# Kernel tuning notes

Hardware: AMD Instinct MI355X
Metric: run time of the kernel (lower is better)

## Reference

```python
import jax, jax.numpy as jnp
import numpy as np

TOKEN_DIM = 192
NUM_HEADS = 4
HEAD_DIM = TOKEN_DIM // NUM_HEADS
TOPK = 128


def _pos_enc(H, W, td):
    # 2D sinusoidal PE identical to GlobalMatcher._get_position_encoding -> [H*W, td]
    y = jnp.repeat(jnp.arange(H, dtype=jnp.float32), W)
    x = jnp.tile(jnp.arange(W, dtype=jnp.float32), H)
    dh = td // 2
    div = jnp.exp(jnp.arange(dh, dtype=jnp.float32) * (-np.log(10000.0) / dh))
    pe_sin = jnp.sin(x[:, None] * div)                       # [N, dh]
    pe_cos = jnp.cos(y[:, None] * div[: td - dh])            # [N, td-dh]
    return jnp.concatenate([pe_sin, pe_cos], axis=1)


def _matcher(feat1, feat2, qw, qb, kw, kb, vw, vb, ow, ob):
    # EfficientGlobalMatcher forward (chunking is a memory detail; math == full topk)
    B, C, H, W = feat1.shape
    N = H * W
    f1 = feat1.reshape(B, C, N).transpose(0, 2, 1)           # [B, N, C]
    f2 = feat2.reshape(B, C, N).transpose(0, 2, 1)
    Q = f1 @ qw + qb                                          # [B, N, td]
    K = f2 @ kw + kb
    V = f2 @ vw + vb
    pe = _pos_enc(H, W, TOKEN_DIM)
    Q = Q + pe[None]
    K = K + pe[None]
    def split(t):  # [B, N, h*d] -> [B, h, N, d]
        return t.reshape(B, N, NUM_HEADS, HEAD_DIM).transpose(0, 2, 1, 3)
    Qh, Kh, Vh = split(Q), split(K), split(V)
    scale = 1.0 / np.sqrt(HEAD_DIM)
    scores = jnp.einsum('bhnd,bhmd->bhnm', Qh, Kh) * scale    # [B, h, N, N]
    k = min(TOPK, N)
    top_vals, top_idx = jax.lax.top_k(scores, k)              # [B, h, N, k]
    attn = jax.nn.softmax(top_vals, axis=-1)
    # gather V rows per (b, h, query, k): [B, h, N, k, d]
    Vg = jnp.take_along_axis(Vh[:, :, None, :, :], top_idx[..., None], axis=3)
    out = jnp.einsum('bhnk,bhnkd->bhnd', attn, Vg)            # [B, h, N, d]
    out = out.transpose(0, 2, 1, 3).reshape(B, N, TOKEN_DIM)
    out = out @ ow + ob
    return out.transpose(0, 2, 1).reshape(B, TOKEN_DIM, H, W)


def setup_inputs() -> dict:
    key = jax.random.key(0)
    dims = [64, 128, 192]
    shapes = [(2, 64, 64, 64), (2, 128, 32, 32), (2, 192, 16, 16)]
    inp = {}
    ks = jax.random.split(key, 32)
    ki = 0
    for lvl, shp in enumerate(shapes):
        inp[f'feat1_{lvl}'] = jax.random.normal(ks[ki], shp, jnp.float32); ki += 1
        inp[f'feat2_{lvl}'] = jax.random.normal(ks[ki], shp, jnp.float32); ki += 1
    for lvl, d in enumerate(dims):
        for nm in ('q', 'k', 'v'):
            inp[f'{nm}w{lvl}'] = jax.random.normal(ks[ki], (d, TOKEN_DIM), jnp.float32) * 0.02; ki += 1
            inp[f'{nm}b{lvl}'] = jnp.zeros((TOKEN_DIM,), jnp.float32)
        inp[f'ow{lvl}'] = jax.random.normal(ks[ki], (TOKEN_DIM, TOKEN_DIM), jnp.float32) * 0.02; ki += 1
        inp[f'ob{lvl}'] = jnp.zeros((TOKEN_DIM,), jnp.float32)
    return inp


def reference(feat1_0, feat2_0, feat1_1, feat2_1, feat1_2, feat2_2,
              qw0, qb0, kw0, kb0, vw0, vb0, ow0, ob0,
              qw1, qb1, kw1, kb1, vw1, vb1, ow1, ob1,
              qw2, qb2, kw2, kb2, vw2, vb2, ow2, ob2):
    t0 = _matcher(feat1_0, feat2_0, qw0, qb0, kw0, kb0, vw0, vb0, ow0, ob0)
    t1 = _matcher(feat1_1, feat2_1, qw1, qb1, kw1, kb1, vw1, vb1, ow1, ob1)
    t2 = _matcher(feat1_2, feat2_2, qw2, qb2, kw2, kb2, vw2, vb2, ow2, ob2)
    return (t0, t1, t2)
```

## Files before the change

### kernel.cpp

```cpp
#include <hip/hip_runtime.h>
#include <math.h>

#define TD 192
#define HD 48
#define KSEL 128
#define QB 4

__device__ __forceinline__ unsigned f2o(float f) {
  unsigned u = __float_as_uint(f);
  return (u & 0x80000000u) ? ~u : (u | 0x80000000u);
}
__device__ __forceinline__ float o2f(unsigned u) {
  unsigned v = (u & 0x80000000u) ? (u & 0x7fffffffu) : ~u;
  return __uint_as_float(v);
}

__global__ void pe_kernel(float* __restrict__ pe, int W) {
  int n = blockIdx.x;
  int t = threadIdx.x;
  const float c = -0.09594104554885301f;
  float val;
  if (t < 96) {
    float dv = expf((float)t * c);
    val = sinf((float)(n % W) * dv);
  } else {
    float dv = expf((float)(t - 96) * c);
    val = cosf((float)(n / W) * dv);
  }
  pe[n * TD + t] = val;
}

__global__ __launch_bounds__(256) void qkv_tiled(
    const float* __restrict__ feat1, const float* __restrict__ feat2,
    const float* __restrict__ qw, const float* __restrict__ qb,
    const float* __restrict__ kw, const float* __restrict__ kb,
    const float* __restrict__ vw, const float* __restrict__ vb,
    const float* __restrict__ pe,
    float* __restrict__ Q, float* __restrict__ Kt, float* __restrict__ V,
    int C, int N) {
  __shared__ float ftile[64][64];
  const int type = blockIdx.y;
  const int tid = threadIdx.x;
  const int gtok = blockIdx.x * 64;
  const int b = gtok / N, n0 = gtok - b * N;
  const float* feat = (type == 0) ? feat1 : feat2;
  const float* wsel = (type == 0) ? qw : (type == 1) ? kw : vw;
  const float* bsel = (type == 0) ? qb : (type == 1) ? kb : vb;
  const int cg = tid >> 4, tg = tid & 15;
  const int ch0 = cg * 12, t0 = tg * 4;

  float4 z = make_float4(0.f, 0.f, 0.f, 0.f);
  float4 a0 = z, a1 = z, a2 = z, a3 = z, a4 = z, a5 = z,
         a6 = z, a7 = z, a8 = z, a9 = z, a10 = z, a11 = z;

  for (int c0 = 0; c0 < C; c0 += 64) {
#pragma unroll
    for (int rep = 0; rep < 4; ++rep) {
      int off = rep * 1024 + tid * 4;
      int r = off >> 6, cc = off & 63;
      *reinterpret_cast<float4*>(&ftile[r][cc]) =
          *reinterpret_cast<const float4*>(&feat[((size_t)(b * C + c0 + r)) * N + n0 + cc]);
    }
    __syncthreads();
#pragma unroll 8
    for (int k = 0; k < 64; ++k) {
      float4 f4 = *reinterpret_cast<const float4*>(&ftile[k][t0]);
      const float* wr = wsel + (size_t)(c0 + k) * TD + ch0;
      float4 w0 = *reinterpret_cast<const float4*>(wr);
      float4 w1 = *reinterpret_cast<const float4*>(wr + 4);
      float4 w2 = *reinterpret_cast<const float4*>(wr + 8);
#define QFMA(A, WS) A.x = fmaf(WS, f4.x, A.x); A.y = fmaf(WS, f4.y, A.y); \
                    A.z = fmaf(WS, f4.z, A.z); A.w = fmaf(WS, f4.w, A.w);
      QFMA(a0, w0.x) QFMA(a1, w0.y) QFMA(a2, w0.z) QFMA(a3, w0.w)
      QFMA(a4, w1.x) QFMA(a5, w1.y) QFMA(a6, w1.z) QFMA(a7, w1.w)
      QFMA(a8, w2.x) QFMA(a9, w2.y) QFMA(a10, w2.z) QFMA(a11, w2.w)
#undef QFMA
    }
    __syncthreads();
  }
  {
    float4 b0 = *reinterpret_cast<const float4*>(&bsel[ch0]);
    float4 b1 = *reinterpret_cast<const float4*>(&bsel[ch0 + 4]);
    float4 b2 = *reinterpret_cast<const float4*>(&bsel[ch0 + 8]);
#define BADD(A, S) A.x += S; A.y += S; A.z += S; A.w += S;
    BADD(a0, b0.x) BADD(a1, b0.y) BADD(a2, b0.z) BADD(a3, b0.w)
    BADD(a4, b1.x) BADD(a5, b1.y) BADD(a6, b1.z) BADD(a7, b1.w)
    BADD(a8, b2.x) BADD(a9, b2.y) BADD(a10, b2.z) BADD(a11, b2.w)
#undef BADD
  }
  if (type < 2) {
#define PEADD(F, TT) { \
    const float* pr = pe + (size_t)(n0 + t0 + (TT)) * TD + ch0; \
    float4 p0 = *reinterpret_cast<const float4*>(pr); \
    float4 p1 = *reinterpret_cast<const float4*>(pr + 4); \
    float4 p2 = *reinterpret_cast<const float4*>(pr + 8); \
    a0.F += p0.x; a1.F += p0.y; a2.F += p0.z; a3.F += p0.w; \
    a4.F += p1.x; a5.F += p1.y; a6.F += p1.z; a7.F += p1.w; \
    a8.F += p2.x; a9.F += p2.y; a10.F += p2.z; a11.F += p2.w; }
    PEADD(x, 0) PEADD(y, 1) PEADD(z, 2) PEADD(w, 3)
#undef PEADD
  }
  if (type == 1) {
#define KSTORE(A, CI) { int ch = ch0 + (CI); int h = ch / HD, d = ch - h * HD; \
    *reinterpret_cast<float4*>(&Kt[((size_t)(b * 4 + h) * HD + d) * N + n0 + t0]) = A; }
    KSTORE(a0, 0) KSTORE(a1, 1) KSTORE(a2, 2) KSTORE(a3, 3)
    KSTORE(a4, 4) KSTORE(a5, 5) KSTORE(a6, 6) KSTORE(a7, 7)
    KSTORE(a8, 8) KSTORE(a9, 9) KSTORE(a10, 10) KSTORE(a11, 11)
#undef KSTORE
  } else {
    float* out = (type == 0) ? Q : V;
#define RSTORE(F, TT) { \
    float* orow = out + (size_t)(b * N + n0 + t0 + (TT)) * TD + ch0; \
    *reinterpret_cast<float4*>(orow)     = make_float4(a0.F, a1.F, a2.F, a3.F); \
    *reinterpret_cast<float4*>(orow + 4) = make_float4(a4.F, a5.F, a6.F, a7.F); \
    *reinterpret_cast<float4*>(orow + 8) = make_float4(a8.F, a9.F, a10.F, a11.F); }
    RSTORE(x, 0) RSTORE(y, 1) RSTORE(z, 2) RSTORE(w, 3)
#undef RSTORE
  }
}

template <int N, int RK, bool FUSE>
__global__ __launch_bounds__(256) void attnA_kernel(
    const float* __restrict__ Q, const float* __restrict__ Kt,
    unsigned* __restrict__ ckey, unsigned short* __restrict__ cidx,
    const float* __restrict__ V, float* __restrict__ O, int bh0) {
  constexpr int R = N / RK;
  constexpr int NV4 = RK / 256;
  constexpr int nq = N / QB;
  constexpr int NCOPY = RK / 256;
  __shared__ unsigned sb[QB * RK];
  __shared__ float qv[QB][HD];

  const int tid = threadIdx.x;
  const int r = blockIdx.x % R;
  const int qg = (blockIdx.x / R) % nq;
  const int bhloc = blockIdx.x / (R * nq);
  const int bh = bh0 + bhloc;
  const int b = bh >> 2, h = bh & 3;
  const int q0 = qg * QB;
  const float scale = 0.14433756729740643f;

  if (tid < QB * HD) {
    int q = tid / HD, d = tid - q * HD;
    qv[q][d] = Q[((size_t)(b * N + q0 + q)) * TD + h * HD + d];
  }
  __syncthreads();

  const int w = tid >> 6, lane = tid & 63;
  const unsigned long long lanelt = (1ull << lane) - 1ull;
  const float* kt = Kt + ((size_t)(b * 4 + h) * HD) * N + r * RK;

  for (int j0 = tid * 4; j0 < RK; j0 += 1024) {
    float4 acc[QB];
#pragma unroll
    for (int q = 0; q < QB; ++q) acc[q] = make_float4(0.f, 0.f, 0.f, 0.f);
#pragma unroll
    for (int d4 = 0; d4 < HD; d4 += 4) {
      float4 k0 = *reinterpret_cast<const float4*>(kt + (size_t)(d4 + 0) * N + j0);
      float4 k1 = *reinterpret_cast<const float4*>(kt + (size_t)(d4 + 1) * N + j0);
      float4 k2 = *reinterpret_cast<const float4*>(kt + (size_t)(d4 + 2) * N + j0);
      float4 k3 = *reinterpret_cast<const float4*>(kt + (size_t)(d4 + 3) * N + j0);
#pragma unroll
      for (int q = 0; q < QB; ++q) {
        float4 qq = *reinterpret_cast<const float4*>(&qv[q][d4]);
        acc[q].x = fmaf(qq.x, k0.x, acc[q].x); acc[q].x = fmaf(qq.y, k1.x, acc[q].x);
        acc[q].x = fmaf(qq.z, k2.x, acc[q].x); acc[q].x = fmaf(qq.w, k3.x, acc[q].x);
        acc[q].y = fmaf(qq.x, k0.y, acc[q].y); acc[q].y = fmaf(qq.y, k1.y, acc[q].y);
        acc[q].y = fmaf(qq.z, k2.y, acc[q].y); acc[q].y = fmaf(qq.w, k3.y, acc[q].y);
        acc[q].z = fmaf(qq.x, k0.z, acc[q].z); acc[q].z = fmaf(qq.y, k1.z, acc[q].z);
        acc[q].z = fmaf(qq.z, k2.z, acc[q].z); acc[q].z = fmaf(qq.w, k3.z, acc[q].z);
        acc[q].w = fmaf(qq.x, k0.w, acc[q].w); acc[q].w = fmaf(qq.y, k1.w, acc[q].w);
        acc[q].w = fmaf(qq.z, k2.w, acc[q].w); acc[q].w = fmaf(qq.w, k3.w, acc[q].w);
      }
    }
#pragma unroll
    for (int q = 0; q < QB; ++q) {
      uint4 kk;
      kk.x = f2o(acc[q].x * scale); kk.y = f2o(acc[q].y * scale);
      kk.z = f2o(acc[q].z * scale); kk.w = f2o(acc[q].w * scale);
      *reinterpret_cast<uint4*>(&sb[q * RK + j0]) = kk;
    }
  }
  __syncthreads();

  uint4 kr[NV4];
#pragma unroll
  for (int i = 0; i < NV4; ++i)
    kr[i] = *reinterpret_cast<const uint4*>(&sb[w * RK + i * 256 + lane * 4]);

  unsigned* h4 = sb + w * RK;
  const unsigned cb = ((unsigned)lane & (NCOPY - 1u)) << 8;
  const unsigned cx = ((unsigned)lane & (NCOPY - 1u)) << 3;

  unsigned kth = 0u, mask = 0u;
  int rem = KSEL;
#pragma unroll
  for (int shift = 24; shift >= 0; shift -= 8) {
#pragma unroll
    for (int i = 0; i < NCOPY; ++i)
      *reinterpret_cast<uint4*>(&h4[i * 256 + lane * 4]) = make_uint4(0, 0, 0, 0);
    if (shift == 24) {
#pragma unroll
      for (int i = 0; i < NV4; ++i) {
        atomicAdd(&h4[cb + (((kr[i].x >> 24)) ^ cx)], 1u);
        atomicAdd(&h4[cb + (((kr[i].y >> 24)) ^ cx)], 1u);
        atomicAdd(&h4[cb + (((kr[i].z >> 24)) ^ cx)], 1u);
        atomicAdd(&h4[cb + (((kr[i].w >> 24)) ^ cx)], 1u);
      }
    } else {
#pragma unroll
      for (int i = 0; i < NV4; ++i) {
        if ((kr[i].x & mask) == kth) atomicAdd(&h4[cb + (((kr[i].x >> shift) & 255u) ^ cx)], 1u);
        if ((kr[i].y & mask) == kth) atomicAdd(&h4[cb + (((kr[i].y >> shift) & 255u) ^ cx)], 1u);
        if ((kr[i].z & mask) == kth) atomicAdd(&h4[cb + (((kr[i].z >> shift) & 255u) ^ cx)], 1u);
        if ((kr[i].w & mask) == kth) atomicAdd(&h4[cb + (((kr[i].w >> shift) & 255u) ^ cx)], 1u);
      }
    }
    int v[4], loc = 0;
#pragma unroll
    for (int i = 0; i < 4; ++i) {
      unsigned bin = (unsigned)(255 - (lane * 4 + i));
      unsigned s = 0;
#pragma unroll
      for (int c = 0; c < NCOPY; ++c) s += h4[c * 256 + (bin ^ ((unsigned)c << 3))];
      v[i] = (int)s;
      loc += v[i];
    }
    int incl = loc;
#pragma unroll
    for (int off = 1; off < 64; off <<= 1) {
      int t = __shfl_up(incl, off, 64);
      if (lane >= off) incl += t;
    }
    int c = incl - loc;
    int selidx = -1, selexcl = 0;
#pragma unroll
    for (int i = 0; i < 4; ++i) {
      if (selidx < 0 && rem > c && rem <= c + v[i]) {
        selidx = 255 - (lane * 4 + i); selexcl = c;
      }
      c += v[i];
    }
    unsigned long long vote = __ballot(selidx >= 0);
    int src = __ffsll((long long)vote) - 1;
    selidx = __shfl(selidx, src, 64);
    selexcl = __shfl(selexcl, src, 64);
    rem -= selexcl;
    kth |= ((unsigned)selidx << shift);
    mask |= (0xFFu << shift);
  }
  const int need_eq = rem;

  if constexpr (FUSE) {
    unsigned mk = 0u;
#pragma unroll
    for (int i = 0; i < NV4; ++i) {
      unsigned a_ = kr[i].x > kr[i].y ? kr[i].x : kr[i].y;
      unsigned b_ = kr[i].z > kr[i].w ? kr[i].z : kr[i].w;
      a_ = a_ > b_ ? a_ : b_; mk = a_ > mk ? a_ : mk;
    }
    for (int off = 32; off > 0; off >>= 1) {
      unsigned o = (unsigned)__shfl_xor((int)mk, off, 64);
      mk = o > mk ? o : mk;
    }
    const float mx = o2f(mk);

    __shared__ int idxb[4][KSEL];
    __shared__ float wb[4][KSEL];
    int selbase = 0, eqbase = 0;
    float lz = 0.f;
#pragma unroll
    for (int i = 0; i < NV4; ++i) {
      const int jb = i * 256 + lane * 4;
      const unsigned u0 = kr[i].x, u1 = kr[i].y, u2 = kr[i].z, u3 = kr[i].w;
      const bool e0 = (u0 == kth), e1 = (u1 == kth), e2 = (u2 == kth), e3 = (u3 == kth);
      const unsigned long long b0 = __ballot(e0), b1 = __ballot(e1), b2 = __ballot(e2), b3 = __ballot(e3);
      const int eqlt = __popcll(b0 & lanelt) + __popcll(b1 & lanelt) + __popcll(b2 & lanelt) + __popcll(b3 & lanelt);
      int eo = 0;
      const bool s0 = (u0 > kth) || (e0 && (eqbase + eqlt + eo) < need_eq); eo += e0 ? 1 : 0;
      const bool s1 = (u1 > kth) || (e1 && (eqbase + eqlt + eo) < need_eq); eo += e1 ? 1 : 0;
      const bool s2 = (u2 > kth) || (e2 && (eqbase + eqlt + eo) < need_eq); eo += e2 ? 1 : 0;
      const bool s3 = (u3 > kth) || (e3 && (eqbase + eqlt + eo) < need_eq); eo += e3 ? 1 : 0;
      const unsigned long long c0 = __ballot(s0), c1 = __ballot(s1), c2 = __ballot(s2), c3 = __ballot(s3);
      const int sellt = __popcll(c0 & lanelt) + __popcll(c1 & lanelt) + __popcll(c2 & lanelt) + __popcll(c3 & lanelt);
      int so = 0;
      if (s0) { int p = selbase + sellt + so; float e = expf(o2f(u0) - mx); idxb[w][p] = jb + 0; wb[w][p] = e; lz += e; } so += s0 ? 1 : 0;
      if (s1) { int p = selbase + sellt + so; float e = expf(o2f(u1) - mx); idxb[w][p] = jb + 1; wb[w][p] = e; lz += e; } so += s1 ? 1 : 0;
      if (s2) { int p = selbase + sellt + so; float e = expf(o2f(u2) - mx); idxb[w][p] = jb + 2; wb[w][p] = e; lz += e; } so += s2 ? 1 : 0;
      if (s3) { int p = selbase + sellt + so; float e = expf(o2f(u3) - mx); idxb[w][p] = jb + 3; wb[w][p] = e; lz += e; } so += s3 ? 1 : 0;
      eqbase += __popcll(b0) + __popcll(b1) + __popcll(b2) + __popcll(b3);
      selbase += __popcll(c0) + __popcll(c1) + __popcll(c2) + __popcll(c3);
    }
    for (int off = 32; off > 0; off >>= 1) lz += __shfl_xor(lz, off, 64);
    const float rz = 1.f / lz;
    if (lane < HD) {
      float acc = 0.f;
#pragma unroll 4
      for (int p = 0; p < KSEL; ++p) {
        acc = fmaf(wb[w][p], V[((size_t)(b * N + idxb[w][p])) * TD + h * HD + lane], acc);
      }
      O[((size_t)(b * N + q0 + w)) * TD + h * HD + lane] = acc * rz;
    }
  } else {
    unsigned* ok = ckey + (((size_t)bhloc * N + q0 + w) * R + r) * KSEL;
    unsigned short* oi = cidx + (((size_t)bhloc * N + q0 + w) * R + r) * KSEL;
    int selbase = 0, eqbase = 0;
#pragma unroll
    for (int i = 0; i < NV4; ++i) {
      const int jb = r * RK + i * 256 + lane * 4;
      const unsigned u0 = kr[i].x, u1 = kr[i].y, u2 = kr[i].z, u3 = kr[i].w;
      const bool e0 = (u0 == kth), e1 = (u1 == kth), e2 = (u2 == kth), e3 = (u3 == kth);
      const unsigned long long b0 = __ballot(e0), b1 = __ballot(e1), b2 = __ballot(e2), b3 = __ballot(e3);
      const int eqlt = __popcll(b0 & lanelt) + __popcll(b1 & lanelt) + __popcll(b2 & lanelt) + __popcll(b3 & lanelt);
      int eo = 0;
      const bool s0 = (u0 > kth) || (e0 && (eqbase + eqlt + eo) < need_eq); eo += e0 ? 1 : 0;
      const bool s1 = (u1 > kth) || (e1 && (eqbase + eqlt + eo) < need_eq); eo += e1 ? 1 : 0;
      const bool s2 = (u2 > kth) || (e2 && (eqbase + eqlt + eo) < need_eq); eo += e2 ? 1 : 0;
      const bool s3 = (u3 > kth) || (e3 && (eqbase + eqlt + eo) < need_eq); eo += e3 ? 1 : 0;
      const unsigned long long c0 = __ballot(s0), c1 = __ballot(s1), c2 = __ballot(s2), c3 = __ballot(s3);
      const int sellt = __popcll(c0 & lanelt) + __popcll(c1 & lanelt) + __popcll(c2 & lanelt) + __popcll(c3 & lanelt);
      int so = 0;
      if (s0) { int p = selbase + sellt + so; ok[p] = u0; oi[p] = (unsigned short)(jb + 0); } so += s0 ? 1 : 0;
      if (s1) { int p = selbase + sellt + so; ok[p] = u1; oi[p] = (unsigned short)(jb + 1); } so += s1 ? 1 : 0;
      if (s2) { int p = selbase + sellt + so; ok[p] = u2; oi[p] = (unsigned short)(jb + 2); } so += s2 ? 1 : 0;
      if (s3) { int p = selbase + sellt + so; ok[p] = u3; oi[p] = (unsigned short)(jb + 3); } so += s3 ? 1 : 0;
      eqbase += __popcll(b0) + __popcll(b1) + __popcll(b2) + __popcll(b3);
      selbase += __popcll(c0) + __popcll(c1) + __popcll(c2) + __popcll(c3);
    }
  }
}

template <int CN>
__global__ __launch_bounds__(256) void attnB_kernel(
    const unsigned* __restrict__ ckey, const unsigned short* __restrict__ cidx,
    const float* __restrict__ V, float* __restrict__ O, int N, int bh0) {
  constexpr int CL = CN / 64;
  __shared__ unsigned hist[4][256];
  __shared__ int idxb[4][KSEL];
  __shared__ float wb[4][KSEL];

  const int tid = threadIdx.x, w = tid >> 6, lane = tid & 63;
  const unsigned long long lanelt = (1ull << lane) - 1ull;
  const int g = blockIdx.x * 4 + w;
  const int bhloc = g / N;
  const int qi = g - bhloc * N;
  const int bh = bh0 + bhloc;
  const int b = bh >> 2, h = bh & 3;

  unsigned ck[CL], ci[CL];
#pragma unroll
  for (int i = 0; i < CL; ++i) {
    ck[i] = ckey[(size_t)g * CN + i * 64 + lane];
    ci[i] = cidx[(size_t)g * CN + i * 64 + lane];
  }

  unsigned mk = 0u;
#pragma unroll
  for (int i = 0; i < CL; ++i) mk = ck[i] > mk ? ck[i] : mk;
  for (int off = 32; off > 0; off >>= 1) {
    unsigned o = (unsigned)__shfl_xor((int)mk, off, 64);
    mk = o > mk ? o : mk;
  }
  const float mx = o2f(mk);

  unsigned* hw = hist[w];
  unsigned kth = 0u, mask = 0u;
  int rem = KSEL;
#pragma unroll
  for (int shift = 24; shift >= 0; shift -= 8) {
#pragma unroll
    for (int i = 0; i < 4; ++i) hw[lane + i * 64] = 0u;
#pragma unroll
    for (int i = 0; i < CL; ++i)
      if ((ck[i] & mask) == kth) atomicAdd(&hw[(ck[i] >> shift) & 255u], 1u);
    int v[4], loc = 0;
#pragma unroll
    for (int i = 0; i < 4; ++i) { v[i] = (int)hw[255 - (lane * 4 + i)]; loc += v[i]; }
    int incl = loc;
#pragma unroll
    for (int off = 1; off < 64; off <<= 1) {
      int t = __shfl_up(incl, off, 64);
      if (lane >= off) incl += t;
    }
    int c = incl - loc;
    int selidx = -1, selexcl = 0;
#pragma unroll
    for (int i = 0; i < 4; ++i) {
      if (selidx < 0 && rem > c && rem <= c + v[i]) {
        selidx = 255 - (lane * 4 + i); selexcl = c;
      }
      c += v[i];
    }
    unsigned long long vote = __ballot(selidx >= 0);
    int src = __ffsll((long long)vote) - 1;
    selidx = __shfl(selidx, src, 64);
    selexcl = __shfl(selexcl, src, 64);
    rem -= selexcl;
    kth |= ((unsigned)selidx << shift);
    mask |= (0xFFu << shift);
  }
  const int need_eq = rem;

  int selbase = 0, eqbase = 0;
  float lz = 0.f;
#pragma unroll
  for (int i = 0; i < CL; ++i) {
    const unsigned u = ck[i];
    const bool eq = (u == kth);
    const unsigned long long beq = __ballot(eq);
    const int eqrank = eqbase + __popcll(beq & lanelt);
    const bool sel = (u > kth) || (eq && eqrank < need_eq);
    const unsigned long long bsel = __ballot(sel);
    const int pos = selbase + __popcll(bsel & lanelt);
    if (sel) {
      float e = expf(o2f(u) - mx);
      idxb[w][pos] = (int)ci[i];
      wb[w][pos] = e;
      lz += e;
    }
    eqbase += __popcll(beq);
    selbase += __popcll(bsel);
  }
  for (int off = 32; off > 0; off >>= 1) lz += __shfl_xor(lz, off, 64);
  const float rz = 1.f / lz;

  if (lane < HD) {
    float acc = 0.f;
#pragma unroll 4
    for (int p = 0; p < KSEL; ++p) {
      acc = fmaf(wb[w][p], V[((size_t)(b * N + idxb[w][p])) * TD + h * HD + lane], acc);
    }
    O[((size_t)(b * N + qi)) * TD + h * HD + lane] = acc * rz;
  }
}

#define OTOK 16
__global__ __launch_bounds__(256) void oproj_kernel(
    const float* __restrict__ O, const float* __restrict__ ow,
    const float* __restrict__ ob, float* __restrict__ out, int N) {
  __shared__ float otile[OTOK][TD + 1];
  const int tid = threadIdx.x;
  const int nt = N / OTOK;
  const int b = blockIdx.x / nt;
  const int n0 = (blockIdx.x % nt) * OTOK;
  const float* obase = O + ((size_t)(b * N + n0)) * TD;
  for (int idx = tid * 4; idx < OTOK * TD; idx += 1024) {
    float4 v = *reinterpret_cast<const float4*>(obase + idx);
    int r = idx / TD, c = idx - r * TD;
    otile[r][c] = v.x; otile[r][c + 1] = v.y; otile[r][c + 2] = v.z; otile[r][c + 3] = v.w;
  }
  __syncthreads();
  const int nl = tid & 15;
  const int ts = (tid >> 4) * 12;
  float a0 = 0.f, a1 = 0.f, a2 = 0.f, a3 = 0.f, a4 = 0.f, a5 = 0.f,
        a6 = 0.f, a7 = 0.f, a8 = 0.f, a9 = 0.f, a10 = 0.f, a11 = 0.f;
  for (int c = 0; c < TD; ++c) {
    float oval = otile[nl][c];
    const float* wr = ow + c * TD + ts;
    float4 w0 = *reinterpret_cast<const float4*>(wr);
    float4 w1 = *reinterpret_cast<const float4*>(wr + 4);
    float4 w2 = *reinterpret_cast<const float4*>(wr + 8);
    a0 = fmaf(oval, w0.x, a0); a1 = fmaf(oval, w0.y, a1);
    a2 = fmaf(oval, w0.z, a2); a3 = fmaf(oval, w0.w, a3);
    a4 = fmaf(oval, w1.x, a4); a5 = fmaf(oval, w1.y, a5);
    a6 = fmaf(oval, w1.z, a6); a7 = fmaf(oval, w1.w, a7);
    a8 = fmaf(oval, w2.x, a8); a9 = fmaf(oval, w2.y, a9);
    a10 = fmaf(oval, w2.z, a10); a11 = fmaf(oval, w2.w, a11);
  }
  const size_t ob2 = ((size_t)b * TD + ts) * N + n0 + nl;
  out[ob2 + 0 * N] = a0 + ob[ts + 0];
  out[ob2 + 1 * N] = a1 + ob[ts + 1];
  out[ob2 + 2 * N] = a2 + ob[ts + 2];
  out[ob2 + 3 * N] = a3 + ob[ts + 3];
  out[ob2 + 4 * N] = a4 + ob[ts + 4];
  out[ob2 + 5 * N] = a5 + ob[ts + 5];
  out[ob2 + 6 * N] = a6 + ob[ts + 6];
  out[ob2 + 7 * N] = a7 + ob[ts + 7];
  out[ob2 + 8 * N] = a8 + ob[ts + 8];
  out[ob2 + 9 * N] = a9 + ob[ts + 9];
  out[ob2 + 10 * N] = a10 + ob[ts + 10];
  out[ob2 + 11 * N] = a11 + ob[ts + 11];
}

extern "C" void kernel_launch(void* const* d_in, const int* in_sizes, int n_in,
                              void* d_out, int out_size, void* d_ws, size_t ws_size,
                              hipStream_t stream) {
  const int B = 2;
  const int Cs[3] = {64, 128, 192};
  const int Hs[3] = {64, 32, 16};
  const size_t out_off[3] = {0,
                             (size_t)2 * TD * 64 * 64,
                             (size_t)2 * TD * 64 * 64 + (size_t)2 * TD * 32 * 32};

  float* ws = (float*)d_ws;
  float* pe = ws;
  float* Q = pe + (size_t)4096 * TD;
  float* Kt = Q + (size_t)B * 4096 * TD;
  float* V = Kt + (size_t)B * 4096 * TD;
  float* Obuf = V + (size_t)B * 4096 * TD;
  unsigned* ckey = (unsigned*)(Obuf + (size_t)B * 4096 * TD);
  unsigned short* cidx = (unsigned short*)(ckey + (size_t)2 * 4096 * 512);

  for (int lvl = 0; lvl < 3; ++lvl) {
    int C = Cs[lvl], H = Hs[lvl], W = H, N = H * W;
    const float* feat1 = (const float*)d_in[lvl * 2 + 0];
    const float* feat2 = (const float*)d_in[lvl * 2 + 1];
    const float* qw = (const float*)d_in[6 + lvl * 8 + 0];
    const float* qb = (const float*)d_in[6 + lvl * 8 + 1];
    const float* kw = (const float*)d_in[6 + lvl * 8 + 2];
    const float* kb = (const float*)d_in[6 + lvl * 8 + 3];
    const float* vw = (const float*)d_in[6 + lvl * 8 + 4];
    const float* vb = (const float*)d_in[6 + lvl * 8 + 5];
    const float* ow = (const float*)d_in[6 + lvl * 8 + 6];
    const float* ob = (const float*)d_in[6 + lvl * 8 + 7];

    pe_kernel<<<N, TD, 0, stream>>>(pe, W);
    dim3 gq(B * N / 64, 3);
    qkv_tiled<<<gq, 256, 0, stream>>>(feat1, feat2, qw, qb, kw, kb, vw, vb, pe, Q, Kt, V, C, N);

    if (N == 4096) {
      for (int g = 0; g < 4; ++g) {
        attnA_kernel<4096, 1024, false><<<8192, 256, 0, stream>>>(
            Q, Kt, ckey, cidx, V, Obuf, g * 2);
        attnB_kernel<512><<<2 * 4096 / 4, 256, 0, stream>>>(
            ckey, cidx, V, Obuf, 4096, g * 2);
      }
    } else if (N == 1024) {
      attnA_kernel<1024, 1024, true><<<8 * 256, 256, 0, stream>>>(
          Q, Kt, ckey, cidx, V, Obuf, 0);
    } else {
      attnA_kernel<256, 256, true><<<8 * 64, 256, 0, stream>>>(
          Q, Kt, ckey, cidx, V, Obuf, 0);
    }
    oproj_kernel<<<B * (N / OTOK), 256, 0, stream>>>(Obuf, ow, ob, (float*)d_out + out_off[lvl], N);
  }
}
```

Measured before the change: 971.0 us.

## Add tie-free fast path to top-k selection, single-copy refine histograms, larger head groups

```diff
diff --git a/kernel.cpp b/kernel.cpp
--- a/kernel.cpp
+++ b/kernel.cpp
@@ -193,38 +193,41 @@
   const unsigned cx = ((unsigned)lane & (NCOPY - 1u)) << 3;
 
   unsigned kth = 0u, mask = 0u;
-  int rem = KSEL;
+  int rem = KSEL, eqcnt = 0;
 #pragma unroll
   for (int shift = 24; shift >= 0; shift -= 8) {
-#pragma unroll
-    for (int i = 0; i < NCOPY; ++i)
-      *reinterpret_cast<uint4*>(&h4[i * 256 + lane * 4]) = make_uint4(0, 0, 0, 0);
+    int v[4], loc = 0;
     if (shift == 24) {
 #pragma unroll
+      for (int i = 0; i < NCOPY; ++i)
+        *reinterpret_cast<uint4*>(&h4[i * 256 + lane * 4]) = make_uint4(0, 0, 0, 0);
+#pragma unroll
       for (int i = 0; i < NV4; ++i) {
-        atomicAdd(&h4[cb + (((kr[i].x >> 24)) ^ cx)], 1u);
-        atomicAdd(&h4[cb + (((kr[i].y >> 24)) ^ cx)], 1u);
-        atomicAdd(&h4[cb + (((kr[i].z >> 24)) ^ cx)], 1u);
-        atomicAdd(&h4[cb + (((kr[i].w >> 24)) ^ cx)], 1u);
+        atomicAdd(&h4[cb + ((kr[i].x >> 24) ^ cx)], 1u);
+        atomicAdd(&h4[cb + ((kr[i].y >> 24) ^ cx)], 1u);
+        atomicAdd(&h4[cb + ((kr[i].z >> 24) ^ cx)], 1u);
+        atomicAdd(&h4[cb + ((kr[i].w >> 24) ^ cx)], 1u);
+      }
+#pragma unroll
+      for (int i = 0; i < 4; ++i) {
+        unsigned bin = (unsigned)(255 - (lane * 4 + i));
+        unsigned s = 0;
+#pragma unroll
+        for (int c = 0; c < NCOPY; ++c) s += h4[c * 256 + (bin ^ ((unsigned)c << 3))];
+        v[i] = (int)s;
+        loc += v[i];
       }
     } else {
+      *reinterpret_cast<uint4*>(&h4[lane * 4]) = make_uint4(0, 0, 0, 0);
 #pragma unroll
       for (int i = 0; i < NV4; ++i) {
-        if ((kr[i].x & mask) == kth) atomicAdd(&h4[cb + (((kr[i].x >> shift) & 255u) ^ cx)], 1u);
-        if ((kr[i].y & mask) == kth) atomicAdd(&h4[cb + (((kr[i].y >> shift) & 255u) ^ cx)], 1u);
-        if ((kr[i].z & mask) == kth) atomicAdd(&h4[cb + (((kr[i].z >> shift) & 255u) ^ cx)], 1u);
-        if ((kr[i].w & mask) == kth) atomicAdd(&h4[cb + (((kr[i].w >> shift) & 255u) ^ cx)], 1u);
-      }
-    }
-    int v[4], loc = 0;
-#pragma unroll
-    for (int i = 0; i < 4; ++i) {
-      unsigned bin = (unsigned)(255 - (lane * 4 + i));
-      unsigned s = 0;
-#pragma unroll
-      for (int c = 0; c < NCOPY; ++c) s += h4[c * 256 + (bin ^ ((unsigned)c << 3))];
-      v[i] = (int)s;
-      loc += v[i];
+        if ((kr[i].x & mask) == kth) atomicAdd(&h4[(kr[i].x >> shift) & 255u], 1u);
+        if ((kr[i].y & mask) == kth) atomicAdd(&h4[(kr[i].y >> shift) & 255u], 1u);
+        if ((kr[i].z & mask) == kth) atomicAdd(&h4[(kr[i].z >> shift) & 255u], 1u);
+        if ((kr[i].w & mask) == kth) atomicAdd(&h4[(kr[i].w >> shift) & 255u], 1u);
+      }
+#pragma unroll
+      for (int i = 0; i < 4; ++i) { v[i] = (int)h4[255 - (lane * 4 + i)]; loc += v[i]; }
     }
     int incl = loc;
 #pragma unroll
@@ -233,11 +236,11 @@
       if (lane >= off) incl += t;
     }
     int c = incl - loc;
-    int selidx = -1, selexcl = 0;
+    int selidx = -1, selexcl = 0, selval = 0;
 #pragma unroll
     for (int i = 0; i < 4; ++i) {
       if (selidx < 0 && rem > c && rem <= c + v[i]) {
-        selidx = 255 - (lane * 4 + i); selexcl = c;
+        selidx = 255 - (lane * 4 + i); selexcl = c; selval = v[i];
       }
       c += v[i];
     }
@@ -245,11 +248,13 @@
     int src = __ffsll((long long)vote) - 1;
     selidx = __shfl(selidx, src, 64);
     selexcl = __shfl(selexcl, src, 64);
+    eqcnt = __shfl(selval, src, 64);
     rem -= selexcl;
     kth |= ((unsigned)selidx << shift);
     mask |= (0xFFu << shift);
   }
   const int need_eq = rem;
+  const bool simple = (eqcnt == need_eq);
 
   if constexpr (FUSE) {
     unsigned mk = 0u;
@@ -267,29 +272,47 @@
 
     __shared__ int idxb[4][KSEL];
     __shared__ float wb[4][KSEL];
-    int selbase = 0, eqbase = 0;
     float lz = 0.f;
-#pragma unroll
-    for (int i = 0; i < NV4; ++i) {
-      const int jb = i * 256 + lane * 4;
-      const unsigned u0 = kr[i].x, u1 = kr[i].y, u2 = kr[i].z, u3 = kr[i].w;
-      const bool e0 = (u0 == kth), e1 = (u1 == kth), e2 = (u2 == kth), e3 = (u3 == kth);
-      const unsigned long long b0 = __ballot(e0), b1 = __ballot(e1), b2 = __ballot(e2), b3 = __ballot(e3);
-      const int eqlt = __popcll(b0 & lanelt) + __popcll(b1 & lanelt) + __popcll(b2 & lanelt) + __popcll(b3 & lanelt);
-      int eo = 0;
-      const bool s0 = (u0 > kth) || (e0 && (eqbase + eqlt + eo) < need_eq); eo += e0 ? 1 : 0;
-      const bool s1 = (u1 > kth) || (e1 && (eqbase + eqlt + eo) < need_eq); eo += e1 ? 1 : 0;
-      const bool s2 = (u2 > kth) || (e2 && (eqbase + eqlt + eo) < need_eq); eo += e2 ? 1 : 0;
-      const bool s3 = (u3 > kth) || (e3 && (eqbase + eqlt + eo) < need_eq); eo += e3 ? 1 : 0;
-      const unsigned long long c0 = __ballot(s0), c1 = __ballot(s1), c2 = __ballot(s2), c3 = __ballot(s3);
-      const int sellt = __popcll(c0 & lanelt) + __popcll(c1 & lanelt) + __popcll(c2 & lanelt) + __popcll(c3 & lanelt);
-      int so = 0;
-      if (s0) { int p = selbase + sellt + so; float e = expf(o2f(u0) - mx); idxb[w][p] = jb + 0; wb[w][p] = e; lz += e; } so += s0 ? 1 : 0;
-      if (s1) { int p = selbase + sellt + so; float e = expf(o2f(u1) - mx); idxb[w][p] = jb + 1; wb[w][p] = e; lz += e; } so += s1 ? 1 : 0;
-      if (s2) { int p = selbase + sellt + so; float e = expf(o2f(u2) - mx); idxb[w][p] = jb + 2; wb[w][p] = e; lz += e; } so += s2 ? 1 : 0;
-      if (s3) { int p = selbase + sellt + so; float e = expf(o2f(u3) - mx); idxb[w][p] = jb + 3; wb[w][p] = e; lz += e; } so += s3 ? 1 : 0;
-      eqbase += __popcll(b0) + __popcll(b1) + __popcll(b2) + __popcll(b3);
-      selbase += __popcll(c0) + __popcll(c1) + __popcll(c2) + __popcll(c3);
+    if (simple) {
+      int selbase = 0;
+#pragma unroll
+      for (int i = 0; i < NV4; ++i) {
+        const int jb = i * 256 + lane * 4;
+        const unsigned u0 = kr[i].x, u1 = kr[i].y, u2 = kr[i].z, u3 = kr[i].w;
+        const bool s0 = (u0 >= kth), s1 = (u1 >= kth), s2 = (u2 >= kth), s3 = (u3 >= kth);
+        const unsigned long long c0 = __ballot(s0), c1 = __ballot(s1), c2 = __ballot(s2), c3 = __ballot(s3);
+        const int sellt = __popcll(c0 & lanelt) + __popcll(c1 & lanelt) + __popcll(c2 & lanelt) + __popcll(c3 & lanelt);
+        int so = 0;
+        if (s0) { int p = selbase + sellt + so; float e = expf(o2f(u0) - mx); idxb[w][p] = jb + 0; wb[w][p] = e; lz += e; } so += s0 ? 1 : 0;
+        if (s1) { int p = selbase + sellt + so; float e = expf(o2f(u1) - mx); idxb[w][p] = jb + 1; wb[w][p] = e; lz += e; } so += s1 ? 1 : 0;
+        if (s2) { int p = selbase + sellt + so; float e = expf(o2f(u2) - mx); idxb[w][p] = jb + 2; wb[w][p] = e; lz += e; } so += s2 ? 1 : 0;
+        if (s3) { int p = selbase + sellt + so; float e = expf(o2f(u3) - mx); idxb[w][p] = jb + 3; wb[w][p] = e; lz += e; } so += s3 ? 1 : 0;
+        selbase += __popcll(c0) + __popcll(c1) + __popcll(c2) + __popcll(c3);
+      }
+    } else {
+      int selbase = 0, eqbase = 0;
+#pragma unroll
+      for (int i = 0; i < NV4; ++i) {
+        const int jb = i * 256 + lane * 4;
+        const unsigned u0 = kr[i].x, u1 = kr[i].y, u2 = kr[i].z, u3 = kr[i].w;
+        const bool e0 = (u0 == kth), e1 = (u1 == kth), e2 = (u2 == kth), e3 = (u3 == kth);
+        const unsigned long long b0 = __ballot(e0), b1 = __ballot(e1), b2 = __ballot(e2), b3 = __ballot(e3);
+        const int eqlt = __popcll(b0 & lanelt) + __popcll(b1 & lanelt) + __popcll(b2 & lanelt) + __popcll(b3 & lanelt);
+        int eo = 0;
+        const bool s0 = (u0 > kth) || (e0 && (eqbase + eqlt + eo) < need_eq); eo += e0 ? 1 : 0;
+        const bool s1 = (u1 > kth) || (e1 && (eqbase + eqlt + eo) < need_eq); eo += e1 ? 1 : 0;
+        const bool s2 = (u2 > kth) || (e2 && (eqbase + eqlt + eo) < need_eq); eo += e2 ? 1 : 0;
+        const bool s3 = (u3 > kth) || (e3 && (eqbase + eqlt + eo) < need_eq); eo += e3 ? 1 : 0;
+        const unsigned long long c0 = __ballot(s0), c1 = __ballot(s1), c2 = __ballot(s2), c3 = __ballot(s3);
+        const int sellt = __popcll(c0 & lanelt) + __popcll(c1 & lanelt) + __popcll(c2 & lanelt) + __popcll(c3 & lanelt);
+        int so = 0;
+        if (s0) { int p = selbase + sellt + so; float e = expf(o2f(u0) - mx); idxb[w][p] = jb + 0; wb[w][p] = e; lz += e; } so += s0 ? 1 : 0;
+        if (s1) { int p = selbase + sellt + so; float e = expf(o2f(u1) - mx); idxb[w][p] = jb + 1; wb[w][p] = e; lz += e; } so += s1 ? 1 : 0;
+        if (s2) { int p = selbase + sellt + so; float e = expf(o2f(u2) - mx); idxb[w][p] = jb + 2; wb[w][p] = e; lz += e; } so += s2 ? 1 : 0;
+        if (s3) { int p = selbase + sellt + so; float e = expf(o2f(u3) - mx); idxb[w][p] = jb + 3; wb[w][p] = e; lz += e; } so += s3 ? 1 : 0;
+        eqbase += __popcll(b0) + __popcll(b1) + __popcll(b2) + __popcll(b3);
+        selbase += __popcll(c0) + __popcll(c1) + __popcll(c2) + __popcll(c3);
+      }
     }
     for (int off = 32; off > 0; off >>= 1) lz += __shfl_xor(lz, off, 64);
     const float rz = 1.f / lz;
@@ -304,28 +327,46 @@
   } else {
     unsigned* ok = ckey + (((size_t)bhloc * N + q0 + w) * R + r) * KSEL;
     unsigned short* oi = cidx + (((size_t)bhloc * N + q0 + w) * R + r) * KSEL;
-    int selbase = 0, eqbase = 0;
-#pragma unroll
-    for (int i = 0; i < NV4; ++i) {
-      const int jb = r * RK + i * 256 + lane * 4;
-      const unsigned u0 = kr[i].x, u1 = kr[i].y, u2 = kr[i].z, u3 = kr[i].w;
-      const bool e0 = (u0 == kth), e1 = (u1 == kth), e2 = (u2 == kth), e3 = (u3 == kth);
-      const unsigned long long b0 = __ballot(e0), b1 = __ballot(e1), b2 = __ballot(e2), b3 = __ballot(e3);
-      const int eqlt = __popcll(b0 & lanelt) + __popcll(b1 & lanelt) + __popcll(b2 & lanelt) + __popcll(b3 & lanelt);
-      int eo = 0;
-      const bool s0 = (u0 > kth) || (e0 && (eqbase + eqlt + eo) < need_eq); eo += e0 ? 1 : 0;
-      const bool s1 = (u1 > kth) || (e1 && (eqbase + eqlt + eo) < need_eq); eo += e1 ? 1 : 0;
-      const bool s2 = (u2 > kth) || (e2 && (eqbase + eqlt + eo) < need_eq); eo += e2 ? 1 : 0;
-      const bool s3 = (u3 > kth) || (e3 && (eqbase + eqlt + eo) < need_eq); eo += e3 ? 1 : 0;
-      const unsigned long long c0 = __ballot(s0), c1 = __ballot(s1), c2 = __ballot(s2), c3 = __ballot(s3);
-      const int sellt = __popcll(c0 & lanelt) + __popcll(c1 & lanelt) + __popcll(c2 & lanelt) + __popcll(c3 & lanelt);
-      int so = 0;
-      if (s0) { int p = selbase + sellt + so; ok[p] = u0; oi[p] = (unsigned short)(jb + 0); } so += s0 ? 1 : 0;
-      if (s1) { int p = selbase + sellt + so; ok[p] = u1; oi[p] = (unsigned short)(jb + 1); } so += s1 ? 1 : 0;
-      if (s2) { int p = selbase + sellt + so; ok[p] = u2; oi[p] = (unsigned short)(jb + 2); } so += s2 ? 1 : 0;
-      if (s3) { int p = selbase + sellt + so; ok[p] = u3; oi[p] = (unsigned short)(jb + 3); } so += s3 ? 1 : 0;
-      eqbase += __popcll(b0) + __popcll(b1) + __popcll(b2) + __popcll(b3);
-      selbase += __popcll(c0) + __popcll(c1) + __popcll(c2) + __popcll(c3);
+    if (simple) {
+      int selbase = 0;
+#pragma unroll
+      for (int i = 0; i < NV4; ++i) {
+        const int jb = r * RK + i * 256 + lane * 4;
+        const unsigned u0 = kr[i].x, u1 = kr[i].y, u2 = kr[i].z, u3 = kr[i].w;
+        const bool s0 = (u0 >= kth), s1 = (u1 >= kth), s2 = (u2 >= kth), s3 = (u3 >= kth);
+        const unsigned long long c0 = __ballot(s0), c1 = __ballot(s1), c2 = __ballot(s2), c3 = __ballot(s3);
+        const int sellt = __popcll(c0 & lanelt) + __popcll(c1 & lanelt) + __popcll(c2 & lanelt) + __popcll(c3 & lanelt);
+        int so = 0;
+        if (s0) { int p = selbase + sellt + so; ok[p] = u0; oi[p] = (unsigned short)(jb + 0); } so += s0 ? 1 : 0;
+        if (s1) { int p = selbase + sellt + so; ok[p] = u1; oi[p] = (unsigned short)(jb + 1); } so += s1 ? 1 : 0;
+        if (s2) { int p = selbase + sellt + so; ok[p] = u2; oi[p] = (unsigned short)(jb + 2); } so += s2 ? 1 : 0;
+        if (s3) { int p = selbase + sellt + so; ok[p] = u3; oi[p] = (unsigned short)(jb + 3); } so += s3 ? 1 : 0;
+        selbase += __popcll(c0) + __popcll(c1) + __popcll(c2) + __popcll(c3);
+      }
+    } else {
+      int selbase = 0, eqbase = 0;
+#pragma unroll
+      for (int i = 0; i < NV4; ++i) {
+        const int jb = r * RK + i * 256 + lane * 4;
+        const unsigned u0 = kr[i].x, u1 = kr[i].y, u2 = kr[i].z, u3 = kr[i].w;
+        const bool e0 = (u0 == kth), e1 = (u1 == kth), e2 = (u2 == kth), e3 = (u3 == kth);
+        const unsigned long long b0 = __ballot(e0), b1 = __ballot(e1), b2 = __ballot(e2), b3 = __ballot(e3);
+        const int eqlt = __popcll(b0 & lanelt) + __popcll(b1 & lanelt) + __popcll(b2 & lanelt) + __popcll(b3 & lanelt);
+        int eo = 0;
+        const bool s0 = (u0 > kth) || (e0 && (eqbase + eqlt + eo) < need_eq); eo += e0 ? 1 : 0;
+        const bool s1 = (u1 > kth) || (e1 && (eqbase + eqlt + eo) < need_eq); eo += e1 ? 1 : 0;
+        const bool s2 = (u2 > kth) || (e2 && (eqbase + eqlt + eo) < need_eq); eo += e2 ? 1 : 0;
+        const bool s3 = (u3 > kth) || (e3 && (eqbase + eqlt + eo) < need_eq); eo += e3 ? 1 : 0;
+        const unsigned long long c0 = __ballot(s0), c1 = __ballot(s1), c2 = __ballot(s2), c3 = __ballot(s3);
+        const int sellt = __popcll(c0 & lanelt) + __popcll(c1 & lanelt) + __popcll(c2 & lanelt) + __popcll(c3 & lanelt);
+        int so = 0;
+        if (s0) { int p = selbase + sellt + so; ok[p] = u0; oi[p] = (unsigned short)(jb + 0); } so += s0 ? 1 : 0;
+        if (s1) { int p = selbase + sellt + so; ok[p] = u1; oi[p] = (unsigned short)(jb + 1); } so += s1 ? 1 : 0;
+        if (s2) { int p = selbase + sellt + so; ok[p] = u2; oi[p] = (unsigned short)(jb + 2); } so += s2 ? 1 : 0;
+        if (s3) { int p = selbase + sellt + so; ok[p] = u3; oi[p] = (unsigned short)(jb + 3); } so += s3 ? 1 : 0;
+        eqbase += __popcll(b0) + __popcll(b1) + __popcll(b2) + __popcll(b3);
+        selbase += __popcll(c0) + __popcll(c1) + __popcll(c2) + __popcll(c3);
+      }
     }
   }
 }
@@ -365,7 +406,7 @@
 
   unsigned* hw = hist[w];
   unsigned kth = 0u, mask = 0u;
-  int rem = KSEL;
+  int rem = KSEL, eqcnt = 0;
 #pragma unroll
   for (int shift = 24; shift >= 0; shift -= 8) {
 #pragma unroll
@@ -383,11 +424,11 @@
       if (lane >= off) incl += t;
     }
     int c = incl - loc;
-    int selidx = -1, selexcl = 0;
+    int selidx = -1, selexcl = 0, selval = 0;
 #pragma unroll
     for (int i = 0; i < 4; ++i) {
       if (selidx < 0 && rem > c && rem <= c + v[i]) {
-        selidx = 255 - (lane * 4 + i); selexcl = c;
+        selidx = 255 - (lane * 4 + i); selexcl = c; selval = v[i];
       }
       c += v[i];
     }
@@ -395,31 +436,51 @@
     int src = __ffsll((long long)vote) - 1;
     selidx = __shfl(selidx, src, 64);
     selexcl = __shfl(selexcl, src, 64);
+    eqcnt = __shfl(selval, src, 64);
     rem -= selexcl;
     kth |= ((unsigned)selidx << shift);
     mask |= (0xFFu << shift);
   }
   const int need_eq = rem;
-
-  int selbase = 0, eqbase = 0;
+  const bool simple = (eqcnt == need_eq);
+
   float lz = 0.f;
-#pragma unroll
-  for (int i = 0; i < CL; ++i) {
-    const unsigned u = ck[i];
-    const bool eq = (u == kth);
-    const unsigned long long beq = __ballot(eq);
-    const int eqrank = eqbase + __popcll(beq & lanelt);
-    const bool sel = (u > kth) || (eq && eqrank < need_eq);
-    const unsigned long long bsel = __ballot(sel);
-    const int pos = selbase + __popcll(bsel & lanelt);
-    if (sel) {
-      float e = expf(o2f(u) - mx);
-      idxb[w][pos] = (int)ci[i];
-      wb[w][pos] = e;
-      lz += e;
-    }
-    eqbase += __popcll(beq);
-    selbase += __popcll(bsel);
+  if (simple) {
+    int selbase = 0;
+#pragma unroll
+    for (int i = 0; i < CL; ++i) {
+      const unsigned u = ck[i];
+      const bool sel = (u >= kth);
+      const unsigned long long bsel = __ballot(sel);
+      const int pos = selbase + __popcll(bsel & lanelt);
+      if (sel) {
+        float e = expf(o2f(u) - mx);
+        idxb[w][pos] = (int)ci[i];
+        wb[w][pos] = e;
+        lz += e;
+      }
+      selbase += __popcll(bsel);
+    }
+  } else {
+    int selbase = 0, eqbase = 0;
+#pragma unroll
+    for (int i = 0; i < CL; ++i) {
+      const unsigned u = ck[i];
+      const bool eq = (u == kth);
+      const unsigned long long beq = __ballot(eq);
+      const int eqrank = eqbase + __popcll(beq & lanelt);
+      const bool sel = (u > kth) || (eq && eqrank < need_eq);
+      const unsigned long long bsel = __ballot(sel);
+      const int pos = selbase + __popcll(bsel & lanelt);
+      if (sel) {
+        float e = expf(o2f(u) - mx);
+        idxb[w][pos] = (int)ci[i];
+        wb[w][pos] = e;
+        lz += e;
+      }
+      eqbase += __popcll(beq);
+      selbase += __popcll(bsel);
+    }
   }
   for (int off = 32; off > 0; off >>= 1) lz += __shfl_xor(lz, off, 64);
   const float rz = 1.f / lz;
@@ -499,7 +560,11 @@
   float* V = Kt + (size_t)B * 4096 * TD;
   float* Obuf = V + (size_t)B * 4096 * TD;
   unsigned* ckey = (unsigned*)(Obuf + (size_t)B * 4096 * TD);
-  unsigned short* cidx = (unsigned short*)(ckey + (size_t)2 * 4096 * 512);
+
+  const size_t base_floats = (size_t)4096 * TD * (1 + 4 * B);
+  const size_t need4 = base_floats * 4 + (size_t)4 * 4096 * 512 * 6 + (1 << 20);
+  const int GBH = (ws_size >= need4) ? 4 : 2;
+  unsigned short* cidx = (unsigned short*)(ckey + (size_t)GBH * 4096 * 512);
 
   for (int lvl = 0; lvl < 3; ++lvl) {
     int C = Cs[lvl], H = Hs[lvl], W = H, N = H * W;
@@ -519,11 +584,11 @@
     qkv_tiled<<<gq, 256, 0, stream>>>(feat1, feat2, qw, qb, kw, kb, vw, vb, pe, Q, Kt, V, C, N);
 
     if (N == 4096) {
-      for (int g = 0; g < 4; ++g) {
-        attnA_kernel<4096, 1024, false><<<8192, 256, 0, stream>>>(
-            Q, Kt, ckey, cidx, V, Obuf, g * 2);
-        attnB_kernel<512><<<2 * 4096 / 4, 256, 0, stream>>>(
-            ckey, cidx, V, Obuf, 4096, g * 2);
+      for (int g = 0; g < 8 / GBH; ++g) {
+        attnA_kernel<4096, 1024, false><<<GBH * 4096, 256, 0, stream>>>(
+            Q, Kt, ckey, cidx, V, Obuf, g * GBH);
+        attnB_kernel<512><<<GBH * 1024, 256, 0, stream>>>(
+            ckey, cidx, V, Obuf, 4096, g * GBH);
       }
     } else if (N == 1024) {
       attnA_kernel<1024, 1024, true><<<8 * 256, 256, 0, stream>>>(
```

New measurement: 891.8 us. -8.2%, faster.
